# Optimization experiments

Measured on AMD Instinct MI355X. Metric: run time of the kernel, lower is better.

Reference implementation:

```python
import jax, jax.numpy as jnp
import numpy as np

B, S, D = 2, 2048, 1024
H, KV, HD = 16, 4, 64
F, E, K = 2816, 8, 2
EPS = 1e-6

def setup_inputs() -> dict:
    key = jax.random.key(0)
    ks = jax.random.split(key, 9)
    def rn(k, shape, std=0.02):
        return jax.random.normal(k, shape, dtype=jnp.float32) * std
    inv_freq = 1.0 / (10000.0 ** (jnp.arange(0, HD, 2, dtype=jnp.float32) / HD))
    freqs = jnp.arange(S, dtype=jnp.float32)[:, None] * inv_freq[None, :]
    emb = jnp.concatenate([freqs, freqs], axis=-1)  # [S, HD]
    return {
        'hidden_states': rn(ks[0], (B, S, D), 1.0),
        'ln1_w': jnp.ones((D,), jnp.float32),
        'ln2_w': jnp.ones((D,), jnp.float32),
        'q_w': rn(ks[1], (H * HD, D)), 'q_b': jnp.zeros((H * HD,), jnp.float32),
        'k_w': rn(ks[2], (KV * HD, D)), 'k_b': jnp.zeros((KV * HD,), jnp.float32),
        'v_w': rn(ks[3], (KV * HD, D)), 'v_b': jnp.zeros((KV * HD,), jnp.float32),
        'o_w': rn(ks[4], (D, H * HD)),
        'router_w': rn(ks[5], (E, D), 0.01),
        'gate_w': rn(ks[6], (E, D, F)),
        'up_w': rn(ks[7], (E, D, F)),
        'down_w': rn(ks[8], (E, F, D)),
        'cos': jnp.cos(emb), 'sin': jnp.sin(emb),
    }

def _rmsnorm(x, w):
    v = jnp.mean(jnp.square(x.astype(jnp.float32)), axis=-1, keepdims=True)
    return (x.astype(jnp.float32) * jax.lax.rsqrt(v + EPS)).astype(x.dtype) * w

def _rotate_half(x):
    h = x.shape[-1] // 2
    return jnp.concatenate([-x[..., h:], x[..., :h]], axis=-1)

def reference(hidden_states, ln1_w, ln2_w, q_w, q_b, k_w, k_b, v_w, v_b, o_w, router_w, gate_w, up_w, down_w, cos, sin):
    # --- attention block (RMSNorm -> Qwen2Attention with RoPE+GQA -> residual) ---
    residual = hidden_states
    h = _rmsnorm(hidden_states, ln1_w)
    q = (h @ q_w.T + q_b).reshape(B, S, H, HD).transpose(0, 2, 1, 3)   # [B,H,S,HD]
    k = (h @ k_w.T + k_b).reshape(B, S, KV, HD).transpose(0, 2, 1, 3)  # [B,KV,S,HD]
    v = (h @ v_w.T + v_b).reshape(B, S, KV, HD).transpose(0, 2, 1, 3)
    c = cos[None, None]; s = sin[None, None]
    q = q * c + _rotate_half(q) * s
    k = k * c + _rotate_half(k) * s
    rep = H // KV
    k = jnp.repeat(k, rep, axis=1)
    v = jnp.repeat(v, rep, axis=1)
    scores = jnp.einsum('bhqd,bhkd->bhqk', q, k) / jnp.sqrt(jnp.float32(HD))
    causal = jnp.tril(jnp.ones((S, S), dtype=bool))
    scores = jnp.where(causal[None, None], scores, jnp.finfo(scores.dtype).min)
    attn = jax.nn.softmax(scores, axis=-1)
    ctx = jnp.einsum('bhqk,bhkd->bhqd', attn, v).transpose(0, 2, 1, 3).reshape(B, S, H * HD)
    x = ctx @ o_w.T + residual
    # --- MoE block (RMSNorm -> router -> expert SwiGLU MLPs -> combine -> residual) ---
    residual = x
    t = _rmsnorm(x, ln2_w).reshape(-1, D)  # [T, D], T = B*S
    logits = t @ router_w.T                # [T, E]
    probs = jax.nn.softmax(logits, axis=-1)
    topk_p, topk_i = jax.lax.top_k(probs, K)
    topk_p = topk_p / jnp.sum(topk_p, axis=-1, keepdims=True)
    # dispatch/combine weights [T,E]: vectorized form of the per-token scatter loop
    w = jnp.sum(jax.nn.one_hot(topk_i, E, dtype=t.dtype) * topk_p[..., None], axis=1)
    aux_loss = jnp.mean(E * jnp.square(jnp.mean(probs, axis=0)))
    out = jnp.zeros_like(t)
    for e in range(E):  # fixed small expert loop
        he = jax.nn.silu(t @ gate_w[e]) * (t @ up_w[e])
        out = out + (he @ down_w[e]) * w[:, e:e + 1]
    x = out.reshape(B, S, D) + residual
    return (x, aux_loss)
```

## Files before the change

### kernel.cpp

```cpp
#include <hip/hip_runtime.h>
#include <hip/hip_bf16.h>

#define DEVI __device__ __forceinline__

typedef float f32x4 __attribute__((ext_vector_type(4)));
typedef _Float16 f16x8 __attribute__((ext_vector_type(8)));
typedef short s16x8 __attribute__((ext_vector_type(8)));
typedef unsigned int u32;

constexpr int Bc = 2, Sc = 2048, Dc = 1024, Hc = 16, KVc = 4, HDc = 64, Fc = 2816, Ec = 8;
constexpr int Tc = Bc * Sc;
constexpr int QKVN = Hc * HDc + 2 * KVc * HDc;
constexpr int CAP = Tc * 2 + Ec * 128;
constexpr float LO_SCALE = 1024.0f;
constexpr float LO_INV = 1.0f / 1024.0f;

DEVI f32x4 mfma16(f16x8 a, f16x8 b, f32x4 c) {
    return __builtin_amdgcn_mfma_f32_16x16x32_f16(a, b, c, 0, 0, 0);
}
DEVI f32x4 mfma16(s16x8 a, s16x8 b, f32x4 c) {
    return __builtin_amdgcn_mfma_f32_16x16x32_bf16(a, b, c, 0, 0, 0);
}

DEVI void gll16(const void *g, void *l) {
    __builtin_amdgcn_global_load_lds(
        (const __attribute__((address_space(1))) u32 *)g,
        (__attribute__((address_space(3))) u32 *)l, 16, 0, 0);
}

DEVI u32 pack2(_Float16 a, _Float16 b) {
    union { _Float16 h[2]; u32 u; } t;
    t.h[0] = a; t.h[1] = b;
    return t.u;
}

template <int N> DEVI void wait_vm() {
    if constexpr (N == 0) asm volatile("s_waitcnt vmcnt(0)" ::: "memory");
    else if constexpr (N == 3) asm volatile("s_waitcnt vmcnt(3)" ::: "memory");
    else if constexpr (N == 4) asm volatile("s_waitcnt vmcnt(4)" ::: "memory");
    else if constexpr (N == 6) asm volatile("s_waitcnt vmcnt(6)" ::: "memory");
    else if constexpr (N == 8) asm volatile("s_waitcnt vmcnt(8)" ::: "memory");
}

template <typename VT> struct FragT;
template <> struct FragT<_Float16> { using type = f16x8; };
template <> struct FragT<__hip_bfloat16> { using type = s16x8; };

struct GemmP {
    const void *Ah, *Al;
    const void *Bh, *Bl, *Bh2;
    long lda, ldb, bExp, K;
    const int *poff, *gidx;
    const float *bias, *resid, *bw;
    float *outF, *outF2;
    __hip_bfloat16 *outBF;
    long ldc;
    int epi;
};

template <typename VT, bool SPLIT, bool GATHER, bool GU, int BN, bool XSWZ = false>
__global__ __launch_bounds__(256, SPLIT ? 3 : ((GU && BN == 128) ? 2 : 4)) void gemm_k(GemmP p) {
    constexpr int BM = 128;
    constexpr int NJ = BN / 32;
    constexpr bool HAS2 = SPLIT || GU;
    constexpr int ACH = SPLIT ? 1024 : 512;
    constexpr int BCH = BN * 4;
    constexpr int NB = HAS2 ? 2 : 1;
    constexpr int TOT = ACH + NB * BCH;
    constexpr int NCH = TOT / 256;
    constexpr int BUFVT = TOT * 8;
    constexpr int AOFF2 = 4096;
    constexpr int BOFF = ACH * 8;
    constexpr int B2OFF = (ACH + BCH) * 8;
    __shared__ __align__(16) VT s[2][BUFVT];
    const int tid = threadIdx.x, lane = tid & 63;
    const int wid = tid >> 6, wm = wid >> 1, wn = wid & 1;
    const int x = lane & 15, hi = lane >> 4;
    int mb = (int)blockIdx.x;
    if constexpr (XSWZ) mb = (mb & 7) * ((int)gridDim.x >> 3) + (mb >> 3);
    long m0 = (long)mb * BM, n0 = (long)blockIdx.y * BN;
    int e = 0;
    if (p.poff) {
        int tot = p.poff[Ec];
        if (m0 >= tot) return;
        while (m0 >= p.poff[e + 1]) ++e;
    }

    const VT *gs[NCH];
    int chd[NCH];
#pragma unroll
    for (int i = 0; i < NCH; ++i) {
        int ch = tid + i * 256;
        chd[i] = ch;
        if (ch < ACH) {
            int slab = ch >> 9, local = ch & 511;
            int r = local >> 2, c = local & 3;
            int cs = c ^ ((r >> 1) & 3);
            long ar = m0 + r;
            if (GATHER) ar = p.gidx[ar];
            const VT *mat = (SPLIT && slab == 1) ? (const VT *)p.Al : (const VT *)p.Ah;
            gs[i] = mat + ar * p.lda + cs * 8;
        } else {
            int idx = ch - ACH;
            int which = idx / BCH, local = idx % BCH;
            int r = local >> 2, c = local & 3;
            int cs = c ^ ((r >> 1) & 3);
            const VT *bmat = (which == 0) ? (const VT *)p.Bh
                           : (SPLIT ? (const VT *)p.Bl : (const VT *)p.Bh2);
            gs[i] = bmat + (long)e * p.bExp + (n0 + r) * p.ldb + cs * 8;
        }
    }

    f32x4 acc[4][NJ];
    f32x4 acc2[HAS2 ? 4 : 1][HAS2 ? NJ : 1];
#pragma unroll
    for (int i = 0; i < 4; ++i)
#pragma unroll
        for (int j = 0; j < NJ; ++j) {
            acc[i][j] = (f32x4){0.f, 0.f, 0.f, 0.f};
            if constexpr (HAS2) acc2[i][j] = (f32x4){0.f, 0.f, 0.f, 0.f};
        }

    using F8 = typename FragT<VT>::type;
    const int KT = (int)(p.K / 32);
    auto stageTo = [&](int kt, int b) {
#pragma unroll
        for (int i = 0; i < NCH; ++i)
            gll16(gs[i] + (long)kt * 32, &s[b][(size_t)chd[i] * 8]);
    };

    stageTo(0, 0);
    if (KT > 1) stageTo(1, 1);

    for (int kt = 0; kt < KT; ++kt) {
        if (kt + 1 < KT) wait_vm<NCH>();
        else wait_vm<0>();
        __builtin_amdgcn_sched_barrier(0);
        __builtin_amdgcn_s_barrier();
        __builtin_amdgcn_sched_barrier(0);
        const int cur = kt & 1;

        F8 afh[4], afl[SPLIT ? 4 : 1];
#pragma unroll
        for (int mi = 0; mi < 4; ++mi) {
            int ar = wm * 64 + mi * 16 + x;
            int ad = (ar * 4 + (hi ^ ((ar >> 1) & 3))) * 8;
            afh[mi] = *(const F8 *)&s[cur][ad];
            if constexpr (SPLIT) afl[mi] = *(const F8 *)&s[cur][AOFF2 + ad];
        }
        __builtin_amdgcn_s_setprio(1);
#pragma unroll
        for (int nj = 0; nj < NJ; ++nj) {
            int br = wn * (BN / 2) + nj * 16 + x;
            int bd = (br * 4 + (hi ^ ((br >> 1) & 3))) * 8;
            F8 bfh = *(const F8 *)&s[cur][BOFF + bd];
            F8 bf2;
            if constexpr (HAS2) bf2 = *(const F8 *)&s[cur][B2OFF + bd];
#pragma unroll
            for (int mi = 0; mi < 4; ++mi) {
                acc[mi][nj] = mfma16(afh[mi], bfh, acc[mi][nj]);
                if constexpr (SPLIT) {
                    acc2[mi][nj] = mfma16(afh[mi], bf2, acc2[mi][nj]);
                    acc2[mi][nj] = mfma16(afl[mi], bfh, acc2[mi][nj]);
                }
                if constexpr (GU) acc2[mi][nj] = mfma16(afh[mi], bf2, acc2[mi][nj]);
            }
        }
        __builtin_amdgcn_s_setprio(0);

        asm volatile("s_waitcnt lgkmcnt(0)" ::: "memory");
        __builtin_amdgcn_sched_barrier(0);
        __builtin_amdgcn_s_barrier();
        __builtin_amdgcn_sched_barrier(0);
        if (kt + 2 < KT) stageTo(kt + 2, cur);
    }

#pragma unroll
    for (int mi = 0; mi < 4; ++mi)
#pragma unroll
        for (int nj = 0; nj < NJ; ++nj)
#pragma unroll
            for (int r = 0; r < 4; ++r) {
                long row = m0 + wm * 64 + mi * 16 + hi * 4 + r;
                long col = n0 + wn * (BN / 2) + nj * 16 + x;
                float v = acc[mi][nj][r];
                if constexpr (GU) {
                    float u = acc2[mi][nj][r];
                    float he = v / (1.f + __expf(-v)) * u;
                    p.outBF[row * p.ldc + col] = __float2bfloat16(he);
                } else {
                    if constexpr (SPLIT) v = fmaf(acc2[mi][nj][r], LO_INV, v);
                    switch (p.epi) {
                    case 0: p.outF[row * p.ldc + col] = v + p.bias[col]; break;
                    case 2: {
                        float o = v + p.resid[row * p.ldc + col];
                        p.outF[row * p.ldc + col] = o;
                        p.outF2[row * p.ldc + col] = o;
                    } break;
                    case 5:
                        p.outF[row * p.ldc + col] = v * p.bw[row];
                        break;
                    }
                }
            }
}

__global__ __launch_bounds__(256) void combine_k(const float *__restrict__ scat,
        const int *__restrict__ tok_slot, float *__restrict__ out) {
    const long tok = blockIdx.x;
    const int c = threadIdx.x * 4;
    const long s0 = tok_slot[tok * 2], s1 = tok_slot[tok * 2 + 1];
    f32x4 a = *(const f32x4 *)(scat + s0 * Dc + c);
    f32x4 b = *(const f32x4 *)(scat + s1 * Dc + c);
    f32x4 o = *(const f32x4 *)(out + tok * Dc + c);
#pragma unroll
    for (int j = 0; j < 4; ++j) o[j] += a[j] + b[j];
    *(f32x4 *)(out + tok * Dc + c) = o;
}

__global__ __launch_bounds__(128, 2) void attn_k(
    const _Float16 *__restrict__ qh, const _Float16 *__restrict__ ql,
    const _Float16 *__restrict__ kh, const _Float16 *__restrict__ kl,
    const _Float16 *__restrict__ vTh, const _Float16 *__restrict__ vTl,
    _Float16 *__restrict__ ctxh, _Float16 *__restrict__ ctxl) {
    __shared__ __align__(16) _Float16 kbuf[2][2][32 * 64];
    __shared__ __align__(16) _Float16 vbuf[2][2][64 * 32];
    const int tid = threadIdx.x, lane = tid & 63, wid = tid >> 6;
    const int x = lane & 15, hi = lane >> 4;
    const int pairI = blockIdx.x;
    const int bh = blockIdx.y;
    const int b = bh >> 4, h = bh & 15, kvh = h >> 2;
    const long kRow0 = (long)b * Sc * 256;
    const long vRow0 = (long)(b * 4 + kvh) * 64 * (long)Sc;

    auto stage = [&](int kt, int bufI) {
        if (wid == 0) {
#pragma unroll
            for (int ss = 0; ss < 2; ++ss) {
                const _Float16 *src = ss ? kl : kh;
#pragma unroll
                for (int i = 0; i < 4; ++i) {
                    int kv = 8 * i + (lane >> 3);
                    int cd = (lane & 7) ^ (kv & 7);
                    const _Float16 *g = src + kRow0 + ((long)kt * 32 + kv) * 256 + kvh * 64 + cd * 8;
                    gll16(g, &kbuf[bufI][ss][i * 512]);
                }
            }
        } else {
#pragma unroll
            for (int ss = 0; ss < 2; ++ss) {
                const _Float16 *src = ss ? vTl : vTh;
#pragma unroll
                for (int i = 0; i < 4; ++i) {
                    int d = 16 * i + (lane >> 2);
                    int ckv = (lane & 3) ^ ((d >> 1) & 3);
                    const _Float16 *g = src + vRow0 + (long)d * Sc + (long)kt * 32 + ckv * 8;
                    gll16(g, &vbuf[bufI][ss][i * 512]);
                }
            }
        }
    };

    for (int seg = 0; seg < 2; ++seg) {
        const int qt = seg ? (63 - pairI) : pairI;
        const int q0 = qt * 32;
        const long qtokW = (long)b * Sc + q0 + wid * 16;

        f16x8 qfh[2], qfl[2];
#pragma unroll
        for (int ks = 0; ks < 2; ++ks) {
            long off = (qtokW + x) * (long)Dc + h * 64 + ks * 32 + hi * 8;
            qfh[ks] = *(const f16x8 *)(qh + off);
            qfl[ks] = *(const f16x8 *)(ql + off);
        }
        asm volatile("s_waitcnt vmcnt(0)" ::: "memory");
        __builtin_amdgcn_sched_barrier(0);

        f32x4 o1[4], o2[4];
        float mrow = -3.0e38f, lrow = 0.f;
#pragma unroll
        for (int dj = 0; dj < 4; ++dj) {
            o1[dj] = (f32x4){0.f, 0.f, 0.f, 0.f};
            o2[dj] = (f32x4){0.f, 0.f, 0.f, 0.f};
        }

        const int NT = qt + 1;

        stage(0, 0);
        stage(1, 1);

        for (int kt = 0; kt < NT; ++kt) {
            if (kt + 1 < NT) asm volatile("s_waitcnt vmcnt(8)" ::: "memory");
            else asm volatile("s_waitcnt vmcnt(0)" ::: "memory");
            __builtin_amdgcn_sched_barrier(0);
            __builtin_amdgcn_s_barrier();
            __builtin_amdgcn_sched_barrier(0);
            const int cur = kt & 1;

            f32x4 s1[2], s2[2];
#pragma unroll
            for (int kvs = 0; kvs < 2; ++kvs) {
                s1[kvs] = (f32x4){0.f, 0.f, 0.f, 0.f};
                s2[kvs] = (f32x4){0.f, 0.f, 0.f, 0.f};
            }
            __builtin_amdgcn_s_setprio(1);
#pragma unroll
            for (int ks = 0; ks < 2; ++ks)
#pragma unroll
                for (int kvs = 0; kvs < 2; ++kvs) {
                    int row = kvs * 16 + x;
                    int addr = row * 64 + (((ks * 4 + hi) ^ (row & 7)) << 3);
                    f16x8 kfh = *(const f16x8 *)&kbuf[cur][0][addr];
                    f16x8 kfl = *(const f16x8 *)&kbuf[cur][1][addr];
                    s1[kvs] = mfma16(kfh, qfh[ks], s1[kvs]);
                    s2[kvs] = mfma16(kfl, qfh[ks], s2[kvs]);
                    s2[kvs] = mfma16(kfh, qfl[ks], s2[kvs]);
                }
            __builtin_amdgcn_s_setprio(0);

            const bool diag = (kt == NT - 1);
            const int qpos = q0 + wid * 16 + x;
            float sv[2][4];
#pragma unroll
            for (int kvs = 0; kvs < 2; ++kvs)
#pragma unroll
                for (int r = 0; r < 4; ++r) {
                    float v = fmaf(s2[kvs][r], LO_INV, s1[kvs][r]) * 0.125f;
                    if (diag) {
                        int kvpos = kt * 32 + kvs * 16 + 4 * hi + r;
                        if (kvpos > qpos) v = -3.0e38f;
                    }
                    sv[kvs][r] = v;
                }
            float mx = sv[0][0];
#pragma unroll
            for (int kvs = 0; kvs < 2; ++kvs)
#pragma unroll
                for (int r = 0; r < 4; ++r) mx = fmaxf(mx, sv[kvs][r]);
            mx = fmaxf(mx, __shfl_xor(mx, 16));
            mx = fmaxf(mx, __shfl_xor(mx, 32));
            if (!__all(mx - mrow <= 8.0f)) {
                float mnew = fmaxf(mrow, mx);
                float scl = __expf(mrow - mnew);
                mrow = mnew;
                lrow *= scl;
                float sclr[4];
#pragma unroll
                for (int r = 0; r < 4; ++r) sclr[r] = __shfl(scl, 4 * hi + r);
#pragma unroll
                for (int dj = 0; dj < 4; ++dj)
#pragma unroll
                    for (int r = 0; r < 4; ++r) {
                        o1[dj][r] *= sclr[r];
                        o2[dj][r] *= sclr[r];
                    }
            }
            float pv[2][4];
            float ls = 0.f;
#pragma unroll
            for (int kvs = 0; kvs < 2; ++kvs)
#pragma unroll
                for (int r = 0; r < 4; ++r) {
                    pv[kvs][r] = __expf(sv[kvs][r] - mrow);
                    ls += pv[kvs][r];
                }
            ls += __shfl_xor(ls, 16);
            ls += __shfl_xor(ls, 32);
            lrow += ls;
            u32 Bh0[2], Bh1[2], Bl0[2], Bl1[2];
#pragma unroll
            for (int pr = 0; pr < 2; ++pr) {
                _Float16 a0 = (_Float16)pv[0][2 * pr], a1 = (_Float16)pv[0][2 * pr + 1];
                _Float16 b0 = (_Float16)pv[1][2 * pr], b1 = (_Float16)pv[1][2 * pr + 1];
                Bh0[pr] = pack2(a0, a1);
                Bh1[pr] = pack2(b0, b1);
                _Float16 la0 = (_Float16)((pv[0][2 * pr] - (float)a0) * LO_SCALE);
                _Float16 la1 = (_Float16)((pv[0][2 * pr + 1] - (float)a1) * LO_SCALE);
                _Float16 lb0 = (_Float16)((pv[1][2 * pr] - (float)b0) * LO_SCALE);
                _Float16 lb1 = (_Float16)((pv[1][2 * pr + 1] - (float)b1) * LO_SCALE);
                Bl0[pr] = pack2(la0, la1);
                Bl1[pr] = pack2(lb0, lb1);
            }
            const int srcLow = x + ((lane & 16) ? 32 : 0);
            const int srcHigh = srcLow + 16;
            const bool useB1 = lane >= 32;
            union { u32 u[4]; f16x8 v; } fh, fl;
#pragma unroll
            for (int pr = 0; pr < 2; ++pr) {
                u32 t0 = (u32)__shfl((int)Bh0[pr], srcLow);
                u32 t1 = (u32)__shfl((int)Bh1[pr], srcLow);
                fh.u[pr] = useB1 ? t1 : t0;
                u32 u0 = (u32)__shfl((int)Bh0[pr], srcHigh);
                u32 u1 = (u32)__shfl((int)Bh1[pr], srcHigh);
                fh.u[2 + pr] = useB1 ? u1 : u0;
                u32 s0 = (u32)__shfl((int)Bl0[pr], srcLow);
                u32 s1v = (u32)__shfl((int)Bl1[pr], srcLow);
                fl.u[pr] = useB1 ? s1v : s0;
                u32 w0 = (u32)__shfl((int)Bl0[pr], srcHigh);
                u32 w1 = (u32)__shfl((int)Bl1[pr], srcHigh);
                fl.u[2 + pr] = useB1 ? w1 : w0;
            }
            f16x8 pah = fh.v, pal = fl.v;

            __builtin_amdgcn_s_setprio(1);
#pragma unroll
            for (int dj = 0; dj < 4; ++dj) {
                int d = dj * 16 + x;
                int addr = d * 32 + ((hi ^ ((d >> 1) & 3)) << 3);
                f16x8 vhf = *(const f16x8 *)&vbuf[cur][0][addr];
                f16x8 vlf = *(const f16x8 *)&vbuf[cur][1][addr];
                o1[dj] = mfma16(pah, vhf, o1[dj]);
                o2[dj] = mfma16(pah, vlf, o2[dj]);
                o2[dj] = mfma16(pal, vhf, o2[dj]);
            }
            __builtin_amdgcn_s_setprio(0);

            asm volatile("s_waitcnt lgkmcnt(0)" ::: "memory");
            __builtin_amdgcn_sched_barrier(0);
            __builtin_amdgcn_s_barrier();
            __builtin_amdgcn_sched_barrier(0);
            if (kt + 2 < NT) stage(kt + 2, cur);
        }

        float linv = 1.0f / lrow;
        float lr[4];
#pragma unroll
        for (int r = 0; r < 4; ++r) lr[r] = __shfl(linv, 4 * hi + r);
#pragma unroll
        for (int dj = 0; dj < 4; ++dj)
#pragma unroll
            for (int r = 0; r < 4; ++r) {
                long tok = qtokW + 4 * hi + r;
                float ov = fmaf(o2[dj][r], LO_INV, o1[dj][r]) * lr[r];
                _Float16 hv = (_Float16)ov;
                long off = tok * Dc + h * 64 + dj * 16 + x;
                ctxh[off] = hv;
                ctxl[off] = (_Float16)((ov - (float)hv) * LO_SCALE);
            }
    }
}

__global__ __launch_bounds__(256) void rmsnorm_split_k(const float *__restrict__ x,
        const float *__restrict__ w, _Float16 *__restrict__ oh, _Float16 *__restrict__ ol) {
    const long row = blockIdx.x;
    const int tid = threadIdx.x, lane = tid & 63, wid = tid >> 6;
    f32x4 v = *(const f32x4 *)(x + row * Dc + tid * 4);
    float ss = v[0] * v[0] + v[1] * v[1] + v[2] * v[2] + v[3] * v[3];
#pragma unroll
    for (int off = 1; off < 64; off <<= 1) ss += __shfl_xor(ss, off);
    __shared__ float sw[4];
    if (lane == 0) sw[wid] = ss;
    __syncthreads();
    float inv = 1.0f / sqrtf((sw[0] + sw[1] + sw[2] + sw[3]) * (1.f / Dc) + 1e-6f);
#pragma unroll
    for (int j = 0; j < 4; ++j) {
        float y = v[j] * inv * w[tid * 4 + j];
        _Float16 hv = (_Float16)y;
        oh[row * Dc + tid * 4 + j] = hv;
        ol[row * Dc + tid * 4 + j] = (_Float16)((y - (float)hv) * LO_SCALE);
    }
}

__global__ __launch_bounds__(256) void rmsnorm2_k(const float *__restrict__ x,
        const float *__restrict__ w, float *__restrict__ tf, __hip_bfloat16 *__restrict__ tb) {
    const long row = blockIdx.x;
    const int tid = threadIdx.x, lane = tid & 63, wid = tid >> 6;
    f32x4 v = *(const f32x4 *)(x + row * Dc + tid * 4);
    float ss = v[0] * v[0] + v[1] * v[1] + v[2] * v[2] + v[3] * v[3];
#pragma unroll
    for (int off = 1; off < 64; off <<= 1) ss += __shfl_xor(ss, off);
    __shared__ float sw[4];
    if (lane == 0) sw[wid] = ss;
    __syncthreads();
    float inv = 1.0f / sqrtf((sw[0] + sw[1] + sw[2] + sw[3]) * (1.f / Dc) + 1e-6f);
#pragma unroll
    for (int j = 0; j < 4; ++j) {
        float y = v[j] * inv * w[tid * 4 + j];
        tf[row * Dc + tid * 4 + j] = y;
        tb[row * Dc + tid * 4 + j] = __float2bfloat16(y);
    }
}

__global__ void split_f16_k(const float *__restrict__ x, _Float16 *hi, _Float16 *lo, long n) {
    for (long i = (long)blockIdx.x * 256 + threadIdx.x; i < n; i += (long)gridDim.x * 256) {
        float v = x[i];
        _Float16 h = (_Float16)v;
        hi[i] = h;
        lo[i] = (_Float16)((v - (float)h) * LO_SCALE);
    }
}

__global__ void pack_qkvw_k(const float *__restrict__ qw, const float *__restrict__ kw,
        const float *__restrict__ vw, _Float16 *wh, _Float16 *wl) {
    const long n = (long)QKVN * Dc;
    for (long i = (long)blockIdx.x * 256 + threadIdx.x; i < n; i += (long)gridDim.x * 256) {
        long o = i >> 10;
        int d = (int)(i & 1023);
        float v;
        if (o < 1024) v = qw[o * 1024 + d];
        else if (o < 1280) v = kw[(o - 1024) * 1024 + d];
        else v = vw[(o - 1280) * 1024 + d];
        _Float16 h = (_Float16)v;
        wh[i] = h;
        wl[i] = (_Float16)((v - (float)h) * LO_SCALE);
    }
}

__global__ void pack_bias_k(const float *qb, const float *kb, const float *vb, float *out) {
    int i = blockIdx.x * 256 + threadIdx.x;
    if (i >= QKVN) return;
    out[i] = (i < 1024) ? qb[i] : (i < 1280) ? kb[i - 1024] : vb[i - 1280];
}

__global__ __launch_bounds__(256) void transpose_bf16_k(const float *__restrict__ in,
        __hip_bfloat16 *__restrict__ out, int R, int C) {
    __shared__ float tile[64 * 65];
    const long eo = (long)blockIdx.z * R * C;
    const int r0 = blockIdx.y * 64, c0 = blockIdx.x * 64;
#pragma unroll
    for (int i = 0; i < 16; ++i) {
        int idx = threadIdx.x + i * 256;
        int r = idx >> 6, c = idx & 63;
        tile[r * 65 + c] = in[eo + (long)(r0 + r) * C + (c0 + c)];
    }
    __syncthreads();
#pragma unroll
    for (int i = 0; i < 16; ++i) {
        int idx = threadIdx.x + i * 256;
        int cc = idx >> 6, rr = idx & 63;
        out[eo + (long)(c0 + cc) * R + (r0 + rr)] = __float2bfloat16(tile[rr * 65 + cc]);
    }
}

__global__ __launch_bounds__(256) void vtrans_k(const float *__restrict__ qkvf,
        _Float16 *__restrict__ vTh, _Float16 *__restrict__ vTl) {
    __shared__ float tile[64][65];
    const int tok0 = blockIdx.x * 64;
    const int bk = blockIdx.y;
    const int b = bk >> 2, kvh = bk & 3;
#pragma unroll
    for (int it = 0; it < 16; ++it) {
        int idx = it * 256 + threadIdx.x;
        int r = idx >> 6, c = idx & 63;
        tile[r][c] = qkvf[((long)b * Sc + tok0 + r) * QKVN + 1280 + kvh * 64 + c];
    }
    __syncthreads();
    const int d = threadIdx.x & 63, ch = threadIdx.x >> 6;
    long orow = ((long)bk * 64 + d) * (long)Sc + tok0 + ch * 16;
    f16x8 oh[2], ol[2];
#pragma unroll
    for (int j = 0; j < 16; ++j) {
        float v = tile[ch * 16 + j][d];
        _Float16 hv = (_Float16)v;
        oh[j >> 3][j & 7] = hv;
        ol[j >> 3][j & 7] = (_Float16)((v - (float)hv) * LO_SCALE);
    }
    *(f16x8 *)(vTh + orow) = oh[0];
    *(f16x8 *)(vTh + orow + 8) = oh[1];
    *(f16x8 *)(vTl + orow) = ol[0];
    *(f16x8 *)(vTl + orow + 8) = ol[1];
}

__global__ __launch_bounds__(256) void rope_k(const float *__restrict__ qkv,
        const float *__restrict__ cosb, const float *__restrict__ sinb,
        _Float16 *qh, _Float16 *ql, _Float16 *kh2, _Float16 *kl2) {
    const long tok = blockIdx.x;
    const int s = (int)(tok % Sc);
    const float *row = qkv + tok * QKVN;
    for (int p = threadIdx.x; p < 640; p += 256) {
        int u = p >> 5, d = p & 31;
        float x1 = row[u * 64 + d], x2 = row[u * 64 + d + 32];
        float cs = cosb[(long)s * 64 + d], sn = sinb[(long)s * 64 + d];
        float o1v = x1 * cs - x2 * sn;
        float o2v = x2 * cs + x1 * sn;
        _Float16 h1 = (_Float16)o1v, h2 = (_Float16)o2v;
        _Float16 l1 = (_Float16)((o1v - (float)h1) * LO_SCALE);
        _Float16 l2 = (_Float16)((o2v - (float)h2) * LO_SCALE);
        if (u < 16) {
            long off = tok * 1024 + u * 64 + d;
            qh[off] = h1; ql[off] = l1; qh[off + 32] = h2; ql[off + 32] = l2;
        } else {
            long off = tok * 256 + (u - 16) * 64 + d;
            kh2[off] = h1; kl2[off] = l1; kh2[off + 32] = h2; kl2[off + 32] = l2;
        }
    }
}

__global__ __launch_bounds__(256) void router_p1_k(const float *__restrict__ t,
        const float *__restrict__ rw, float *probs, int *tok_e, float *tok_w, int *cnt) {
    const int tid = threadIdx.x, lane = tid & 63, wid = tid >> 6;
    const long tok = (long)blockIdx.x * 4 + wid;
    const float *row = t + tok * Dc;
    const int d0 = lane * 16;
    f32x4 xv[4];
#pragma unroll
    for (int i = 0; i < 4; ++i) xv[i] = *(const f32x4 *)(row + d0 + i * 4);
    float acc[8];
#pragma unroll
    for (int e = 0; e < 8; ++e) {
        const float *wr = rw + (long)e * Dc + d0;
        float a = 0.f;
#pragma unroll
        for (int i = 0; i < 4; ++i) {
            f32x4 wv = *(const f32x4 *)(wr + i * 4);
            a += xv[i][0] * wv[0] + xv[i][1] * wv[1] + xv[i][2] * wv[2] + xv[i][3] * wv[3];
        }
        acc[e] = a;
    }
#pragma unroll
    for (int off = 1; off < 64; off <<= 1)
#pragma unroll
        for (int e = 0; e < 8; ++e) acc[e] += __shfl_xor(acc[e], off);
    if (lane == 0) {
        float mx = acc[0];
#pragma unroll
        for (int e = 1; e < 8; ++e) mx = fmaxf(mx, acc[e]);
        float ex[8], s = 0.f;
#pragma unroll
        for (int e = 0; e < 8; ++e) { ex[e] = expf(acc[e] - mx); s += ex[e]; }
        float inv = 1.f / s;
        int i1 = -1, i2 = -1;
        float p1v = -1.f, p2v = -1.f;
#pragma unroll
        for (int e = 0; e < 8; ++e) {
            float pe = ex[e] * inv;
            probs[tok * 8 + e] = pe;
            if (pe > p1v) { i2 = i1; p2v = p1v; i1 = e; p1v = pe; }
            else if (pe > p2v) { i2 = e; p2v = pe; }
        }
        float wsum = p1v + p2v;
        tok_e[tok * 2] = i1; tok_e[tok * 2 + 1] = i2;
        tok_w[tok * 2] = p1v / wsum; tok_w[tok * 2 + 1] = p2v / wsum;
        atomicAdd(&cnt[i1], 1);
        atomicAdd(&cnt[i2], 1);
    }
}

__global__ __launch_bounds__(1024) void router_p2_k(const int *cnt, const float *probs,
        int *poff, float *aux_out) {
    __shared__ float sd[1024];
    const int tid = threadIdx.x;
    const int e = tid & 7, rs = tid >> 3;
    float s = 0.f;
    for (int r = rs; r < Tc; r += 128) s += probs[(long)r * 8 + e];
    sd[tid] = s;
    __syncthreads();
    for (int st = 64; st >= 1; st >>= 1) {
        if (rs < st) sd[tid] += sd[tid + st * 8];
        __syncthreads();
    }
    if (tid == 0) {
        float a = 0.f;
        for (int ee = 0; ee < 8; ++ee) {
            float m = sd[ee] * (1.f / Tc);
            a += m * m;
        }
        aux_out[0] = a;
        int o = 0;
        poff[0] = 0;
        for (int ee = 0; ee < 8; ++ee) { o += (cnt[ee] + 127) & ~127; poff[ee + 1] = o; }
    }
}

__global__ void router_p3_k(const int *tok_e, const float *tok_w, const int *poff,
        int *cursor, int *btok, float *bw, int *tok_slot) {
    long tok = (long)blockIdx.x * 256 + threadIdx.x;
    if (tok >= Tc) return;
#pragma unroll
    for (int j = 0; j < 2; ++j) {
        int e = tok_e[tok * 2 + j];
        int slot = atomicAdd(&cursor[e], 1);
        btok[poff[e] + slot] = (int)tok;
        bw[poff[e] + slot] = tok_w[tok * 2 + j];
        tok_slot[tok * 2 + j] = poff[e] + slot;
    }
}

__global__ void router_p4_k(const int *poff, const int *cnt, int *btok, float *bw) {
    int s = blockIdx.x * 256 + threadIdx.x;
    if (s >= poff[8]) return;
    int e = 0;
    while (s >= poff[e + 1]) ++e;
    if (s - poff[e] >= cnt[e]) { btok[s] = 0; bw[s] = 0.f; }
}

extern "C" void kernel_launch(void *const *d_in, const int *in_sizes, int n_in,
                              void *d_out, int out_size, void *d_ws, size_t ws_size,
                              hipStream_t stream) {
    (void)in_sizes; (void)n_in;
    const float *hidden = (const float *)d_in[0];
    const float *ln1 = (const float *)d_in[1];
    const float *ln2 = (const float *)d_in[2];
    const float *qw = (const float *)d_in[3];
    const float *qb = (const float *)d_in[4];
    const float *kw = (const float *)d_in[5];
    const float *kb = (const float *)d_in[6];
    const float *vw = (const float *)d_in[7];
    const float *vb = (const float *)d_in[8];
    const float *ow = (const float *)d_in[9];
    const float *rw = (const float *)d_in[10];
    const float *gw = (const float *)d_in[11];
    const float *uw = (const float *)d_in[12];
    const float *dwn = (const float *)d_in[13];
    const float *cosb = (const float *)d_in[14];
    const float *sinb = (const float *)d_in[15];
    float *outx = (float *)d_out;

    char *base = (char *)d_ws;
    size_t off = 0;
    auto alloc = [&](size_t bytes) -> char * {
        char *p = base + off;
        off += (bytes + 255) & ~(size_t)255;
        return p;
    };
    _Float16 *qkvwh = (_Float16 *)alloc((size_t)QKVN * Dc * 2);
    _Float16 *qkvwl = (_Float16 *)alloc((size_t)QKVN * Dc * 2);
    float *qkvb = (float *)alloc(QKVN * 4);
    _Float16 *owh = (_Float16 *)alloc((size_t)Dc * Dc * 2);
    _Float16 *owl = (_Float16 *)alloc((size_t)Dc * Dc * 2);
    __hip_bfloat16 *gateT = (__hip_bfloat16 *)alloc((size_t)Ec * Fc * Dc * 2);
    __hip_bfloat16 *upT = (__hip_bfloat16 *)alloc((size_t)Ec * Fc * Dc * 2);
    __hip_bfloat16 *downT = (__hip_bfloat16 *)alloc((size_t)Ec * Dc * Fc * 2);
    char *U2 = alloc((size_t)Tc * Dc * 4);
    _Float16 *hh = (_Float16 *)U2;
    _Float16 *hl = hh + (size_t)Tc * Dc;
    float *tf = (float *)U2;
    char *U3 = alloc((size_t)Tc * Dc * 4);
    _Float16 *qhb = (_Float16 *)U3;
    _Float16 *qlb = qhb + (size_t)Tc * Dc;
    float *x1 = (float *)U3;
    _Float16 *khb = (_Float16 *)alloc((size_t)Tc * 256 * 2);
    _Float16 *klb = (_Float16 *)alloc((size_t)Tc * 256 * 2);
    _Float16 *vTh = (_Float16 *)alloc((size_t)Tc * 256 * 2);
    _Float16 *vTl = (_Float16 *)alloc((size_t)Tc * 256 * 2);
    float *scat = (float *)U2;
    _Float16 *ctxh = (_Float16 *)alloc((size_t)Tc * Dc * 2);
    _Float16 *ctxl = (_Float16 *)alloc((size_t)Tc * Dc * 2);
    __hip_bfloat16 *tbf = (__hip_bfloat16 *)alloc((size_t)Tc * Dc * 2);
    float *probs = (float *)alloc((size_t)Tc * 8 * 4);
    int *tok_e = (int *)alloc((size_t)Tc * 2 * 4);
    float *tok_w = (float *)alloc((size_t)Tc * 2 * 4);
    int *tok_slot = (int *)alloc((size_t)Tc * 2 * 4);
    int *cnt = (int *)alloc(256);
    int *cursor = cnt + 8;
    int *poff = (int *)alloc(256);
    int *btok = (int *)alloc((size_t)CAP * 4);
    float *bwgt = (float *)alloc((size_t)CAP * 4);
    size_t qkvfB = (size_t)Tc * QKVN * 4;
    size_t gbufB = (size_t)CAP * Fc * 2;
    size_t u1B = qkvfB > gbufB ? qkvfB : gbufB;
    char *U1 = alloc(u1B);
    float *qkvf = (float *)U1;
    __hip_bfloat16 *gbuf = (__hip_bfloat16 *)U1;

    if (off > ws_size) {
        hipMemsetAsync(d_out, 0, (size_t)out_size * 4, stream);
        return;
    }

    hipMemsetAsync(cnt, 0, 64, stream);
    pack_qkvw_k<<<1024, 256, 0, stream>>>(qw, kw, vw, qkvwh, qkvwl);
    pack_bias_k<<<(QKVN + 255) / 256, 256, 0, stream>>>(qb, kb, vb, qkvb);
    split_f16_k<<<1024, 256, 0, stream>>>(ow, owh, owl, (long)Dc * Dc);
    transpose_bf16_k<<<dim3(Fc / 64, Dc / 64, Ec), 256, 0, stream>>>(gw, gateT, Dc, Fc);
    transpose_bf16_k<<<dim3(Fc / 64, Dc / 64, Ec), 256, 0, stream>>>(uw, upT, Dc, Fc);
    transpose_bf16_k<<<dim3(Dc / 64, Fc / 64, Ec), 256, 0, stream>>>(dwn, downT, Fc, Dc);
    rmsnorm_split_k<<<Tc, 256, 0, stream>>>(hidden, ln1, hh, hl);

    GemmP g{};
    g.Ah = hh; g.Al = hl; g.Bh = qkvwh; g.Bl = qkvwl;
    g.lda = Dc; g.ldb = Dc; g.bExp = 0; g.K = Dc;
    g.bias = qkvb; g.outF = qkvf; g.ldc = QKVN; g.epi = 0;
    gemm_k<_Float16, true, false, false, 64><<<dim3(Tc / 128, QKVN / 64), 256, 0, stream>>>(g);

    rope_k<<<Tc, 256, 0, stream>>>(qkvf, cosb, sinb, qhb, qlb, khb, klb);
    vtrans_k<<<dim3(Sc / 64, Bc * KVc), 256, 0, stream>>>(qkvf, vTh, vTl);
    attn_k<<<dim3(Sc / 64, Bc * Hc), 128, 0, stream>>>(qhb, qlb, khb, klb, vTh, vTl, ctxh, ctxl);

    GemmP go{};
    go.Ah = ctxh; go.Al = ctxl; go.Bh = owh; go.Bl = owl;
    go.lda = Dc; go.ldb = Dc; go.bExp = 0; go.K = Dc;
    go.resid = hidden; go.outF = x1; go.outF2 = outx; go.ldc = Dc; go.epi = 2;
    gemm_k<_Float16, true, false, false, 64><<<dim3(Tc / 128, Dc / 64), 256, 0, stream>>>(go);

    rmsnorm2_k<<<Tc, 256, 0, stream>>>(x1, ln2, tf, tbf);
    router_p1_k<<<Tc / 4, 256, 0, stream>>>(tf, rw, probs, tok_e, tok_w, cnt);
    router_p2_k<<<1, 1024, 0, stream>>>(cnt, probs, poff, outx + (long)Tc * Dc);
    router_p3_k<<<Tc / 256, 256, 0, stream>>>(tok_e, tok_w, poff, cursor, btok, bwgt, tok_slot);
    router_p4_k<<<CAP / 256, 256, 0, stream>>>(poff, cnt, btok, bwgt);

    GemmP gg{};
    gg.Ah = tbf; gg.Bh = gateT; gg.Bh2 = upT;
    gg.lda = Dc; gg.ldb = Dc; gg.bExp = (long)Fc * Dc; gg.K = Dc;
    gg.poff = poff; gg.gidx = btok; gg.outBF = gbuf; gg.ldc = Fc;
    gemm_k<__hip_bfloat16, false, true, true, 128, true><<<dim3(CAP / 128, Fc / 128), 256, 0, stream>>>(gg);

    GemmP gd{};
    gd.Ah = gbuf; gd.Bh = downT;
    gd.lda = Fc; gd.ldb = Fc; gd.bExp = (long)Dc * Fc; gd.K = Fc;
    gd.poff = poff; gd.bw = bwgt;
    gd.outF = scat; gd.ldc = Dc; gd.epi = 5;
    gemm_k<__hip_bfloat16, false, false, false, 128, true><<<dim3(CAP / 128, Dc / 128), 256, 0, stream>>>(gd);

    combine_k<<<Tc, 256, 0, stream>>>(scat, tok_slot, outx);
}
```

Before: 692.2 us.

## Widen attention blocks to 64 query rows and use BN=128 split GEMMs

The attention kernel moves from 2 to 4 waves per block, each covering 16 query rows, so a block handles a 64-row query tile. Loading of K/V hi/lo tiles is spread over all four waves, and the waves owning the first 32 rows skip the last KV tile. The QKV and output-projection split-f16 GEMMs switch to 128-wide N tiles, and launch bounds are derived from the LDS footprint. The intent is more K/V reuse per load and fewer GEMM blocks, at the cost of lower occupancy and fewer blocks in flight.

```diff
diff --git a/kernel.cpp b/kernel.cpp
--- a/kernel.cpp
+++ b/kernel.cpp
@@ -40,11 +40,20 @@
     else if constexpr (N == 4) asm volatile("s_waitcnt vmcnt(4)" ::: "memory");
     else if constexpr (N == 6) asm volatile("s_waitcnt vmcnt(6)" ::: "memory");
     else if constexpr (N == 8) asm volatile("s_waitcnt vmcnt(8)" ::: "memory");
+    else if constexpr (N == 12) asm volatile("s_waitcnt vmcnt(12)" ::: "memory");
 }
 
 template <typename VT> struct FragT;
 template <> struct FragT<_Float16> { using type = f16x8; };
 template <> struct FragT<__hip_bfloat16> { using type = s16x8; };
+
+template <bool SPLIT, bool GU, int BN>
+constexpr int lbBlocks() {
+    int tot = (SPLIT ? 1024 : 512) + ((SPLIT || GU) ? 2 : 1) * BN * 4;
+    int ldsB = tot * 32;
+    int blocks = (160 * 1024) / ldsB;
+    return blocks > 4 ? 4 : blocks;
+}
 
 struct GemmP {
     const void *Ah, *Al;
@@ -59,7 +68,7 @@
 };
 
 template <typename VT, bool SPLIT, bool GATHER, bool GU, int BN, bool XSWZ = false>
-__global__ __launch_bounds__(256, SPLIT ? 3 : ((GU && BN == 128) ? 2 : 4)) void gemm_k(GemmP p) {
+__global__ __launch_bounds__(256, (lbBlocks<SPLIT, GU, BN>())) void gemm_k(GemmP p) {
     constexpr int BM = 128;
     constexpr int NJ = BN / 32;
     constexpr bool HAS2 = SPLIT || GU;
@@ -218,7 +227,7 @@
     *(f32x4 *)(out + tok * Dc + c) = o;
 }
 
-__global__ __launch_bounds__(128, 2) void attn_k(
+__global__ __launch_bounds__(256, 4) void attn_k(
     const _Float16 *__restrict__ qh, const _Float16 *__restrict__ ql,
     const _Float16 *__restrict__ kh, const _Float16 *__restrict__ kl,
     const _Float16 *__restrict__ vTh, const _Float16 *__restrict__ vTl,
@@ -234,36 +243,30 @@
     const long vRow0 = (long)(b * 4 + kvh) * 64 * (long)Sc;
 
     auto stage = [&](int kt, int bufI) {
-        if (wid == 0) {
-#pragma unroll
-            for (int ss = 0; ss < 2; ++ss) {
-                const _Float16 *src = ss ? kl : kh;
-#pragma unroll
-                for (int i = 0; i < 4; ++i) {
-                    int kv = 8 * i + (lane >> 3);
-                    int cd = (lane & 7) ^ (kv & 7);
-                    const _Float16 *g = src + kRow0 + ((long)kt * 32 + kv) * 256 + kvh * 64 + cd * 8;
-                    gll16(g, &kbuf[bufI][ss][i * 512]);
-                }
+        if (wid < 2) {
+            const _Float16 *src = (wid == 1) ? kl : kh;
+#pragma unroll
+            for (int i = 0; i < 4; ++i) {
+                int kv = 8 * i + (lane >> 3);
+                int cd = (lane & 7) ^ (kv & 7);
+                const _Float16 *g = src + kRow0 + ((long)kt * 32 + kv) * 256 + kvh * 64 + cd * 8;
+                gll16(g, &kbuf[bufI][wid][i * 512]);
             }
         } else {
-#pragma unroll
-            for (int ss = 0; ss < 2; ++ss) {
-                const _Float16 *src = ss ? vTl : vTh;
-#pragma unroll
-                for (int i = 0; i < 4; ++i) {
-                    int d = 16 * i + (lane >> 2);
-                    int ckv = (lane & 3) ^ ((d >> 1) & 3);
-                    const _Float16 *g = src + vRow0 + (long)d * Sc + (long)kt * 32 + ckv * 8;
-                    gll16(g, &vbuf[bufI][ss][i * 512]);
-                }
+            const _Float16 *src = (wid == 3) ? vTl : vTh;
+#pragma unroll
+            for (int i = 0; i < 4; ++i) {
+                int d = 16 * i + (lane >> 2);
+                int ckv = (lane & 3) ^ ((d >> 1) & 3);
+                const _Float16 *g = src + vRow0 + (long)d * Sc + (long)kt * 32 + ckv * 8;
+                gll16(g, &vbuf[bufI][wid - 2][i * 512]);
             }
         }
     };
 
     for (int seg = 0; seg < 2; ++seg) {
-        const int qt = seg ? (63 - pairI) : pairI;
-        const int q0 = qt * 32;
+        const int qt = seg ? (31 - pairI) : pairI;
+        const int q0 = qt * 64;
         const long qtokW = (long)b * Sc + q0 + wid * 16;
 
         f16x8 qfh[2], qfl[2];
@@ -284,136 +287,139 @@
             o2[dj] = (f32x4){0.f, 0.f, 0.f, 0.f};
         }
 
-        const int NT = qt + 1;
+        const int NT = 2 * qt + 2;
+        const int myNT = NT - (wid < 2 ? 1 : 0);
 
         stage(0, 0);
         stage(1, 1);
 
         for (int kt = 0; kt < NT; ++kt) {
-            if (kt + 1 < NT) asm volatile("s_waitcnt vmcnt(8)" ::: "memory");
+            if (kt + 1 < NT) asm volatile("s_waitcnt vmcnt(4)" ::: "memory");
             else asm volatile("s_waitcnt vmcnt(0)" ::: "memory");
             __builtin_amdgcn_sched_barrier(0);
             __builtin_amdgcn_s_barrier();
             __builtin_amdgcn_sched_barrier(0);
             const int cur = kt & 1;
 
-            f32x4 s1[2], s2[2];
-#pragma unroll
-            for (int kvs = 0; kvs < 2; ++kvs) {
-                s1[kvs] = (f32x4){0.f, 0.f, 0.f, 0.f};
-                s2[kvs] = (f32x4){0.f, 0.f, 0.f, 0.f};
+            if (kt < myNT) {
+                f32x4 s1[2], s2[2];
+#pragma unroll
+                for (int kvs = 0; kvs < 2; ++kvs) {
+                    s1[kvs] = (f32x4){0.f, 0.f, 0.f, 0.f};
+                    s2[kvs] = (f32x4){0.f, 0.f, 0.f, 0.f};
+                }
+                __builtin_amdgcn_s_setprio(1);
+#pragma unroll
+                for (int ks = 0; ks < 2; ++ks)
+#pragma unroll
+                    for (int kvs = 0; kvs < 2; ++kvs) {
+                        int row = kvs * 16 + x;
+                        int addr = row * 64 + (((ks * 4 + hi) ^ (row & 7)) << 3);
+                        f16x8 kfh = *(const f16x8 *)&kbuf[cur][0][addr];
+                        f16x8 kfl = *(const f16x8 *)&kbuf[cur][1][addr];
+                        s1[kvs] = mfma16(kfh, qfh[ks], s1[kvs]);
+                        s2[kvs] = mfma16(kfl, qfh[ks], s2[kvs]);
+                        s2[kvs] = mfma16(kfh, qfl[ks], s2[kvs]);
+                    }
+                __builtin_amdgcn_s_setprio(0);
+
+                const bool diag = (kt == myNT - 1);
+                const int qpos = q0 + wid * 16 + x;
+                float sv[2][4];
+#pragma unroll
+                for (int kvs = 0; kvs < 2; ++kvs)
+#pragma unroll
+                    for (int r = 0; r < 4; ++r) {
+                        float v = fmaf(s2[kvs][r], LO_INV, s1[kvs][r]) * 0.125f;
+                        if (diag) {
+                            int kvpos = kt * 32 + kvs * 16 + 4 * hi + r;
+                            if (kvpos > qpos) v = -3.0e38f;
+                        }
+                        sv[kvs][r] = v;
+                    }
+                float mx = sv[0][0];
+#pragma unroll
+                for (int kvs = 0; kvs < 2; ++kvs)
+#pragma unroll
+                    for (int r = 0; r < 4; ++r) mx = fmaxf(mx, sv[kvs][r]);
+                mx = fmaxf(mx, __shfl_xor(mx, 16));
+                mx = fmaxf(mx, __shfl_xor(mx, 32));
+                if (!__all(mx - mrow <= 8.0f)) {
+                    float mnew = fmaxf(mrow, mx);
+                    float scl = __expf(mrow - mnew);
+                    mrow = mnew;
+                    lrow *= scl;
+                    float sclr[4];
+#pragma unroll
+                    for (int r = 0; r < 4; ++r) sclr[r] = __shfl(scl, 4 * hi + r);
+#pragma unroll
+                    for (int dj = 0; dj < 4; ++dj)
+#pragma unroll
+                        for (int r = 0; r < 4; ++r) {
+                            o1[dj][r] *= sclr[r];
+                            o2[dj][r] *= sclr[r];
+                        }
+                }
+                float pv[2][4];
+                float ls = 0.f;
+#pragma unroll
+                for (int kvs = 0; kvs < 2; ++kvs)
+#pragma unroll
+                    for (int r = 0; r < 4; ++r) {
+                        pv[kvs][r] = __expf(sv[kvs][r] - mrow);
+                        ls += pv[kvs][r];
+                    }
+                ls += __shfl_xor(ls, 16);
+                ls += __shfl_xor(ls, 32);
+                lrow += ls;
+                u32 Bh0[2], Bh1[2], Bl0[2], Bl1[2];
+#pragma unroll
+                for (int pr = 0; pr < 2; ++pr) {
+                    _Float16 a0 = (_Float16)pv[0][2 * pr], a1 = (_Float16)pv[0][2 * pr + 1];
+                    _Float16 b0 = (_Float16)pv[1][2 * pr], b1 = (_Float16)pv[1][2 * pr + 1];
+                    Bh0[pr] = pack2(a0, a1);
+                    Bh1[pr] = pack2(b0, b1);
+                    _Float16 la0 = (_Float16)((pv[0][2 * pr] - (float)a0) * LO_SCALE);
+                    _Float16 la1 = (_Float16)((pv[0][2 * pr + 1] - (float)a1) * LO_SCALE);
+                    _Float16 lb0 = (_Float16)((pv[1][2 * pr] - (float)b0) * LO_SCALE);
+                    _Float16 lb1 = (_Float16)((pv[1][2 * pr + 1] - (float)b1) * LO_SCALE);
+                    Bl0[pr] = pack2(la0, la1);
+                    Bl1[pr] = pack2(lb0, lb1);
+                }
+                const int srcLow = x + ((lane & 16) ? 32 : 0);
+                const int srcHigh = srcLow + 16;
+                const bool useB1 = lane >= 32;
+                union { u32 u[4]; f16x8 v; } fh, fl;
+#pragma unroll
+                for (int pr = 0; pr < 2; ++pr) {
+                    u32 t0 = (u32)__shfl((int)Bh0[pr], srcLow);
+                    u32 t1 = (u32)__shfl((int)Bh1[pr], srcLow);
+                    fh.u[pr] = useB1 ? t1 : t0;
+                    u32 u0 = (u32)__shfl((int)Bh0[pr], srcHigh);
+                    u32 u1 = (u32)__shfl((int)Bh1[pr], srcHigh);
+                    fh.u[2 + pr] = useB1 ? u1 : u0;
+                    u32 s0 = (u32)__shfl((int)Bl0[pr], srcLow);
+                    u32 s1v = (u32)__shfl((int)Bl1[pr], srcLow);
+                    fl.u[pr] = useB1 ? s1v : s0;
+                    u32 w0 = (u32)__shfl((int)Bl0[pr], srcHigh);
+                    u32 w1 = (u32)__shfl((int)Bl1[pr], srcHigh);
+                    fl.u[2 + pr] = useB1 ? w1 : w0;
+                }
+                f16x8 pah = fh.v, pal = fl.v;
+
+                __builtin_amdgcn_s_setprio(1);
+#pragma unroll
+                for (int dj = 0; dj < 4; ++dj) {
+                    int d = dj * 16 + x;
+                    int addr = d * 32 + ((hi ^ ((d >> 1) & 3)) << 3);
+                    f16x8 vhf = *(const f16x8 *)&vbuf[cur][0][addr];
+                    f16x8 vlf = *(const f16x8 *)&vbuf[cur][1][addr];
+                    o1[dj] = mfma16(pah, vhf, o1[dj]);
+                    o2[dj] = mfma16(pah, vlf, o2[dj]);
+                    o2[dj] = mfma16(pal, vhf, o2[dj]);
+                }
+                __builtin_amdgcn_s_setprio(0);
             }
-            __builtin_amdgcn_s_setprio(1);
-#pragma unroll
-            for (int ks = 0; ks < 2; ++ks)
-#pragma unroll
-                for (int kvs = 0; kvs < 2; ++kvs) {
-                    int row = kvs * 16 + x;
-                    int addr = row * 64 + (((ks * 4 + hi) ^ (row & 7)) << 3);
-                    f16x8 kfh = *(const f16x8 *)&kbuf[cur][0][addr];
-                    f16x8 kfl = *(const f16x8 *)&kbuf[cur][1][addr];
-                    s1[kvs] = mfma16(kfh, qfh[ks], s1[kvs]);
-                    s2[kvs] = mfma16(kfl, qfh[ks], s2[kvs]);
-                    s2[kvs] = mfma16(kfh, qfl[ks], s2[kvs]);
-                }
-            __builtin_amdgcn_s_setprio(0);
-
-            const bool diag = (kt == NT - 1);
-            const int qpos = q0 + wid * 16 + x;
-            float sv[2][4];
-#pragma unroll
-            for (int kvs = 0; kvs < 2; ++kvs)
-#pragma unroll
-                for (int r = 0; r < 4; ++r) {
-                    float v = fmaf(s2[kvs][r], LO_INV, s1[kvs][r]) * 0.125f;
-                    if (diag) {
-                        int kvpos = kt * 32 + kvs * 16 + 4 * hi + r;
-                        if (kvpos > qpos) v = -3.0e38f;
-                    }
-                    sv[kvs][r] = v;
-                }
-            float mx = sv[0][0];
-#pragma unroll
-            for (int kvs = 0; kvs < 2; ++kvs)
-#pragma unroll
-                for (int r = 0; r < 4; ++r) mx = fmaxf(mx, sv[kvs][r]);
-            mx = fmaxf(mx, __shfl_xor(mx, 16));
-            mx = fmaxf(mx, __shfl_xor(mx, 32));
-            if (!__all(mx - mrow <= 8.0f)) {
-                float mnew = fmaxf(mrow, mx);
-                float scl = __expf(mrow - mnew);
-                mrow = mnew;
-                lrow *= scl;
-                float sclr[4];
-#pragma unroll
-                for (int r = 0; r < 4; ++r) sclr[r] = __shfl(scl, 4 * hi + r);
-#pragma unroll
-                for (int dj = 0; dj < 4; ++dj)
-#pragma unroll
-                    for (int r = 0; r < 4; ++r) {
-                        o1[dj][r] *= sclr[r];
-                        o2[dj][r] *= sclr[r];
-                    }
-            }
-            float pv[2][4];
-            float ls = 0.f;
-#pragma unroll
-            for (int kvs = 0; kvs < 2; ++kvs)
-#pragma unroll
-                for (int r = 0; r < 4; ++r) {
-                    pv[kvs][r] = __expf(sv[kvs][r] - mrow);
-                    ls += pv[kvs][r];
-                }
-            ls += __shfl_xor(ls, 16);
-            ls += __shfl_xor(ls, 32);
-            lrow += ls;
-            u32 Bh0[2], Bh1[2], Bl0[2], Bl1[2];
-#pragma unroll
-            for (int pr = 0; pr < 2; ++pr) {
-                _Float16 a0 = (_Float16)pv[0][2 * pr], a1 = (_Float16)pv[0][2 * pr + 1];
-                _Float16 b0 = (_Float16)pv[1][2 * pr], b1 = (_Float16)pv[1][2 * pr + 1];
-                Bh0[pr] = pack2(a0, a1);
-                Bh1[pr] = pack2(b0, b1);
-                _Float16 la0 = (_Float16)((pv[0][2 * pr] - (float)a0) * LO_SCALE);
-                _Float16 la1 = (_Float16)((pv[0][2 * pr + 1] - (float)a1) * LO_SCALE);
-                _Float16 lb0 = (_Float16)((pv[1][2 * pr] - (float)b0) * LO_SCALE);
-                _Float16 lb1 = (_Float16)((pv[1][2 * pr + 1] - (float)b1) * LO_SCALE);
-                Bl0[pr] = pack2(la0, la1);
-                Bl1[pr] = pack2(lb0, lb1);
-            }
-            const int srcLow = x + ((lane & 16) ? 32 : 0);
-            const int srcHigh = srcLow + 16;
-            const bool useB1 = lane >= 32;
-            union { u32 u[4]; f16x8 v; } fh, fl;
-#pragma unroll
-            for (int pr = 0; pr < 2; ++pr) {
-                u32 t0 = (u32)__shfl((int)Bh0[pr], srcLow);
-                u32 t1 = (u32)__shfl((int)Bh1[pr], srcLow);
-                fh.u[pr] = useB1 ? t1 : t0;
-                u32 u0 = (u32)__shfl((int)Bh0[pr], srcHigh);
-                u32 u1 = (u32)__shfl((int)Bh1[pr], srcHigh);
-                fh.u[2 + pr] = useB1 ? u1 : u0;
-                u32 s0 = (u32)__shfl((int)Bl0[pr], srcLow);
-                u32 s1v = (u32)__shfl((int)Bl1[pr], srcLow);
-                fl.u[pr] = useB1 ? s1v : s0;
-                u32 w0 = (u32)__shfl((int)Bl0[pr], srcHigh);
-                u32 w1 = (u32)__shfl((int)Bl1[pr], srcHigh);
-                fl.u[2 + pr] = useB1 ? w1 : w0;
-            }
-            f16x8 pah = fh.v, pal = fl.v;
-
-            __builtin_amdgcn_s_setprio(1);
-#pragma unroll
-            for (int dj = 0; dj < 4; ++dj) {
-                int d = dj * 16 + x;
-                int addr = d * 32 + ((hi ^ ((d >> 1) & 3)) << 3);
-                f16x8 vhf = *(const f16x8 *)&vbuf[cur][0][addr];
-                f16x8 vlf = *(const f16x8 *)&vbuf[cur][1][addr];
-                o1[dj] = mfma16(pah, vhf, o1[dj]);
-                o2[dj] = mfma16(pah, vlf, o2[dj]);
-                o2[dj] = mfma16(pal, vhf, o2[dj]);
-            }
-            __builtin_amdgcn_s_setprio(0);
 
             asm volatile("s_waitcnt lgkmcnt(0)" ::: "memory");
             __builtin_amdgcn_sched_barrier(0);
@@ -771,17 +777,17 @@
     g.Ah = hh; g.Al = hl; g.Bh = qkvwh; g.Bl = qkvwl;
     g.lda = Dc; g.ldb = Dc; g.bExp = 0; g.K = Dc;
     g.bias = qkvb; g.outF = qkvf; g.ldc = QKVN; g.epi = 0;
-    gemm_k<_Float16, true, false, false, 64><<<dim3(Tc / 128, QKVN / 64), 256, 0, stream>>>(g);
+    gemm_k<_Float16, true, false, false, 128><<<dim3(Tc / 128, QKVN / 128), 256, 0, stream>>>(g);
 
     rope_k<<<Tc, 256, 0, stream>>>(qkvf, cosb, sinb, qhb, qlb, khb, klb);
     vtrans_k<<<dim3(Sc / 64, Bc * KVc), 256, 0, stream>>>(qkvf, vTh, vTl);
-    attn_k<<<dim3(Sc / 64, Bc * Hc), 128, 0, stream>>>(qhb, qlb, khb, klb, vTh, vTl, ctxh, ctxl);
+    attn_k<<<dim3(16, Bc * Hc), 256, 0, stream>>>(qhb, qlb, khb, klb, vTh, vTl, ctxh, ctxl);
 
     GemmP go{};
     go.Ah = ctxh; go.Al = ctxl; go.Bh = owh; go.Bl = owl;
     go.lda = Dc; go.ldb = Dc; go.bExp = 0; go.K = Dc;
     go.resid = hidden; go.outF = x1; go.outF2 = outx; go.ldc = Dc; go.epi = 2;
-    gemm_k<_Float16, true, false, false, 64><<<dim3(Tc / 128, Dc / 64), 256, 0, stream>>>(go);
+    gemm_k<_Float16, true, false, false, 128><<<dim3(Tc / 128, Dc / 128), 256, 0, stream>>>(go);
 
     rmsnorm2_k<<<Tc, 256, 0, stream>>>(x1, ln2, tf, tbf);
     router_p1_k<<<Tc / 4, 256, 0, stream>>>(tf, rw, probs, tok_e, tok_w, cnt);
```

Result: slower. 841.9 us (+21.6%).
